# Kernel tuning notes

Measured on AMD Instinct MI355X. Metric: run time of the kernel, lower is better.

## Reference

```python
import jax, jax.numpy as jnp
import numpy as np

N = 20000      # nodes
E = 320000     # edges (avg degree 16)
DIN = 512
DOUT = 512


def setup_inputs() -> dict:
    key = jax.random.key(0)
    ks = jax.random.split(key, 20)
    inp = {}
    inp["X"] = jax.random.normal(ks[0], (N, DIN), jnp.float32)
    inp["edge_index"] = jax.random.randint(ks[1], (2, E), 0, N)
    inp["edge_weight"] = jax.random.uniform(ks[2], (E,), jnp.float32, minval=0.1, maxval=1.0)
    inp["H"] = jax.random.normal(ks[3], (N, DOUT), jnp.float32)
    # six GCNConv layers: x-convs [DIN,DOUT], h-convs [DOUT,DOUT], each with bias [DOUT]
    specs = [("xz", DIN), ("hz", DOUT), ("xr", DIN), ("hr", DOUT), ("xh", DIN), ("hh", DOUT)]
    for i, (tag, din) in enumerate(specs):
        inp[f"W_{tag}"] = jax.random.normal(ks[4 + 2 * i], (din, DOUT), jnp.float32) * 0.05
        inp[f"b_{tag}"] = jax.random.normal(ks[5 + 2 * i], (DOUT,), jnp.float32) * 0.01
    return inp


def _gcn_norm(edge_index, edge_weight, n):
    # PyG gcn_norm: add self-loops (weight 1), symmetric D^-1/2 A D^-1/2
    row, col = edge_index[0], edge_index[1]
    loop = jnp.arange(n, dtype=row.dtype)
    row = jnp.concatenate([row, loop])
    col = jnp.concatenate([col, loop])
    w = jnp.concatenate([edge_weight, jnp.ones((n,), edge_weight.dtype)])
    deg = jax.ops.segment_sum(w, col, num_segments=n)
    dinv = jnp.where(deg > 0, jax.lax.rsqrt(jnp.where(deg > 0, deg, 1.0)), 0.0)
    norm = dinv[row] * w * dinv[col]
    return row, col, norm


def _gcn_conv(x, W, b, row, col, norm, n):
    # out[i] = sum_{j->i} norm_e * (x W)[j] + b
    xw = x @ W                               # [N, DOUT] dense GEMM
    msg = norm[:, None] * xw[row]            # [E+N, DOUT] gather
    return jax.ops.segment_sum(msg, col, num_segments=n) + b


def reference(X, edge_index, edge_weight, H,
              W_xz, b_xz, W_hz, b_hz,
              W_xr, b_xr, W_hr, b_hr,
              W_xh, b_xh, W_hh, b_hh):
    n = X.shape[0]
    row, col, norm = _gcn_norm(edge_index, edge_weight, n)
    conv = lambda x, W, b: _gcn_conv(x, W, b, row, col, norm, n)
    Z = jax.nn.sigmoid(conv(X, W_xz, b_xz) + conv(H, W_hz, b_hz))
    R = jax.nn.sigmoid(conv(X, W_xr, b_xr) + conv(H, W_hr, b_hr))
    H_tilde = jnp.tanh(conv(X, W_xh, b_xh) + conv(H * R, W_hh, b_hh))
    return Z * H + (1.0 - Z) * H_tilde
```

## Files before the change

### kernel.cpp

```cpp
#include <hip/hip_runtime.h>

#define NN 20000
#define NP 20096
#define NE 320000
#define DD 512

typedef __bf16 bf16x8 __attribute__((ext_vector_type(8)));
typedef float f32x4 __attribute__((ext_vector_type(4)));
typedef float f32x2 __attribute__((ext_vector_type(2)));
typedef unsigned short u16;

__device__ __forceinline__ float sigmoidf_(float x) {
  return __builtin_amdgcn_rcpf(1.f + __expf(-x));
}
__device__ __forceinline__ float tanhf_(float x) {
  float xc = fminf(fmaxf(x, -15.f), 15.f);
  float u = __expf(2.f * xc);
  return (u - 1.f) * __builtin_amdgcn_rcpf(u + 1.f);
}

__device__ __forceinline__ unsigned bf16pair(float a, float b) {
  unsigned ua = __builtin_bit_cast(unsigned, a);
  unsigned ub = __builtin_bit_cast(unsigned, b);
  ua = (ua + 0x7FFFu + ((ua >> 16) & 1u)) >> 16;
  ub = (ub + 0x7FFFu + ((ub >> 16) & 1u)) >> 16;
  return ua | (ub << 16);
}
__device__ __forceinline__ u16 bf16one(float a) {
  unsigned ua = __builtin_bit_cast(unsigned, a);
  return (u16)((ua + 0x7FFFu + ((ua >> 16) & 1u)) >> 16);
}
__device__ __forceinline__ float bflo(unsigned w) { return __builtin_bit_cast(float, w << 16); }
__device__ __forceinline__ float bfhi(unsigned w) { return __builtin_bit_cast(float, w & 0xFFFF0000u); }
__device__ __forceinline__ float bf2f(u16 v) { return __builtin_bit_cast(float, (unsigned)v << 16); }

__device__ __forceinline__ void gload16(const void* g, void* l) {
  __builtin_amdgcn_global_load_lds(
      (const __attribute__((address_space(1))) unsigned int*)g,
      (__attribute__((address_space(3))) unsigned int*)l, 16, 0, 0);
}

#define CVT_B 10000
#define INIT_B 79
#define WT_B 1536
__global__ __launch_bounds__(256) void k_setup(
    const float* __restrict__ X, const float* __restrict__ H,
    u16* __restrict__ Xb, u16* __restrict__ Hb,
    const float* __restrict__ W0, const float* __restrict__ W1,
    const float* __restrict__ W2, const float* __restrict__ W3,
    const float* __restrict__ W4, const float* __restrict__ W5,
    u16* __restrict__ T, float* __restrict__ deg, int* __restrict__ cnt) {
  __shared__ float t[32][33];
  int b = blockIdx.x;
  if (b < CVT_B) {
    const int n8 = NN * DD / 8;
    int i = b * 256 + threadIdx.x;
    const float* src = (i < n8) ? X : H;
    u16* dst = (i < n8) ? Xb : Hb;
    int k = (i < n8) ? i : i - n8;
    const float4* s = (const float4*)src;
    float4 v0 = s[k * 2], v1 = s[k * 2 + 1];
    uint4 o = {bf16pair(v0.x, v0.y), bf16pair(v0.z, v0.w),
               bf16pair(v1.x, v1.y), bf16pair(v1.z, v1.w)};
    ((uint4*)dst)[k] = o;
  } else if (b < CVT_B + INIT_B) {
    int i = (b - CVT_B) * 256 + threadIdx.x;
    if (i < NN) { deg[i] = 1.0f; cnt[i] = 0; }
  } else {
    int wb = b - CVT_B - INIT_B;
    const float* Wsrc;
    switch (wb >> 8) {
      case 0: Wsrc = W0; break; case 1: Wsrc = W1; break; case 2: Wsrc = W2; break;
      case 3: Wsrc = W3; break; case 4: Wsrc = W4; break; default: Wsrc = W5; break;
    }
    u16* Wt = T + (size_t)(wb >> 8) * 262144;
    int rb = wb & 255;
    int kb = (rb & 15) * 32, nb = (rb >> 4) * 32;
    int tx = threadIdx.x & 31, ty = threadIdx.x >> 5;
#pragma unroll
    for (int i2 = 0; i2 < 4; ++i2)
      t[ty * 4 + i2][tx] = Wsrc[(size_t)(kb + ty * 4 + i2) * 512 + nb + tx];
    __syncthreads();
#pragma unroll
    for (int i2 = 0; i2 < 4; ++i2)
      Wt[(size_t)(nb + ty * 4 + i2) * 512 + kb + tx] = bf16one(t[tx][ty * 4 + i2]);
  }
}

__global__ void k_accum(const int* col, const float* w, float* deg, int* cnt) {
  int e = blockIdx.x * 256 + threadIdx.x;
  if (e < NE) {
    int c = col[e];
    atomicAdd(&deg[c], w[e]);
    atomicAdd(&cnt[c], 1);
  }
}

__global__ void k_scan(const int* cnt, int* ptr, int* pos) {
  __shared__ int sdata[1024];
  const int ITEMS = (NN + 1023) / 1024;
  int tid = threadIdx.x;
  int base = tid * ITEMS;
  int s = 0;
  for (int j = 0; j < ITEMS; ++j) { int i = base + j; if (i < NN) s += cnt[i]; }
  sdata[tid] = s;
  __syncthreads();
  for (int off = 1; off < 1024; off <<= 1) {
    int v = 0;
    if (tid >= off) v = sdata[tid - off];
    __syncthreads();
    sdata[tid] += v;
    __syncthreads();
  }
  int run = (tid == 0) ? 0 : sdata[tid - 1];
  for (int j = 0; j < ITEMS; ++j) {
    int i = base + j;
    if (i < NN) { ptr[i] = run; pos[i] = run; run += cnt[i]; }
  }
  if (tid == 0) ptr[NN] = NE;
}

__global__ void k_scatter(const int* row, const int* col, const float* w, const float* deg,
                          int* pos, int* erow, float* enorm) {
  int e = blockIdx.x * 256 + threadIdx.x;
  if (e < NE) {
    int r = row[e], c = col[e];
    int slot = atomicAdd(&pos[c], 1);
    erow[slot] = r;
    enorm[slot] = rsqrtf(deg[r]) * w[e] * rsqrtf(deg[c]);
  }
}

#define AGG_B 10000
__global__ __launch_bounds__(256) void k_agg_one(const u16* __restrict__ SA,
                                                 const u16* __restrict__ SB,
                                                 u16* __restrict__ DA,
                                                 u16* __restrict__ DB,
                                                 const int* __restrict__ ptr,
                                                 const int* __restrict__ erow,
                                                 const float* __restrict__ enorm,
                                                 const float* __restrict__ deg) {
  int bid = blockIdx.x;
  bool second = bid >= AGG_B;
  const uint4* S4 = (const uint4*)(second ? SB : SA);
  uint4* D4 = (uint4*)(second ? DB : DA);
  int b = second ? bid - AGG_B : bid;
  int slice = b & 7, nb = b >> 3;
  int w = threadIdx.x >> 6, lane = threadIdx.x & 63;
  int node = nb * 16 + w * 4 + (lane >> 4);
  int q = lane & 15;
  int g = q >> 3, cl = q & 7;
  int soff = slice * 8 + cl;

  float s = rsqrtf(deg[node]), s2 = s * s;
  int pe = ptr[node], e1 = ptr[node + 1];

  f32x2 ax[4] = {};
  auto accum = [&](float nm, uint4 xv) {
    unsigned xw[4] = {xv.x, xv.y, xv.z, xv.w};
    f32x2 nm2 = {nm, nm};
#pragma unroll
    for (int j = 0; j < 4; ++j) {
      f32x2 xf = {bflo(xw[j]), bfhi(xw[j])};
      ax[j] += nm2 * xf;
    }
  };

  if (g == 0) accum(s2, S4[(size_t)node * 64 + soff]);
  int e = pe + 1 - g;
  for (; e + 6 < e1; e += 8) {
    int r0 = erow[e];     float n0 = enorm[e];
    int r1 = erow[e + 2]; float n1 = enorm[e + 2];
    int r2 = erow[e + 4]; float n2 = enorm[e + 4];
    int r3 = erow[e + 6]; float n3 = enorm[e + 6];
    uint4 x0 = S4[(size_t)r0 * 64 + soff];
    uint4 x1 = S4[(size_t)r1 * 64 + soff];
    uint4 x2 = S4[(size_t)r2 * 64 + soff];
    uint4 x3 = S4[(size_t)r3 * 64 + soff];
    accum(n0, x0);
    accum(n1, x1);
    accum(n2, x2);
    accum(n3, x3);
  }
  for (; e < e1; e += 2) accum(enorm[e], S4[(size_t)erow[e] * 64 + soff]);

#pragma unroll
  for (int j = 0; j < 4; ++j) {
    ax[j].x += __shfl_xor(ax[j].x, 8, 64);
    ax[j].y += __shfl_xor(ax[j].y, 8, 64);
  }

  if (g == 0) {
    uint4 ox = {bf16pair(ax[0].x, ax[0].y), bf16pair(ax[1].x, ax[1].y),
                bf16pair(ax[2].x, ax[2].y), bf16pair(ax[3].x, ax[3].y)};
    D4[(size_t)node * 64 + soff] = ox;
  }
}

__global__ __launch_bounds__(256) void k_gemm_big(
    const u16* __restrict__ AXb, const u16* __restrict__ AHb,
    const u16* __restrict__ WtAll,
    const float* __restrict__ bxz, const float* __restrict__ bhz,
    const float* __restrict__ bxr, const float* __restrict__ bhr,
    const u16* __restrict__ Hb,
    u16* __restrict__ Zb, u16* __restrict__ HRb) {
  __shared__ unsigned char smem[32768];
  const int tid = threadIdx.x;
  const int lane = tid & 63, w = tid >> 6;
  const int wr = w >> 1, wc = w & 1;

  const int q = 157;
  const int xcd = blockIdx.x & 7, ii = blockIdx.x >> 3;
  const int wk = xcd * q + ii;
  const int rowBase = (wk >> 3) * 128;
  const int c = wk & 7;
  const int seg = c >> 2;
  const int colBase = (c & 3) * 128;

  const u16* W1 = WtAll + (size_t)(seg ? 2 : 0) * 262144;
  const u16* W2 = WtAll + (size_t)(seg ? 3 : 1) * 262144;

  f32x4 acc[4][4] = {};

  const int lrow = lane & 15;
  const int lkb = (lane >> 4) << 4;
  const int swz = (lane & 7) << 4;
  const int srow = w * 32 + (lane >> 3);
  const int scol = (((lane & 7) ^ (lane >> 3)) << 4);

  for (int pass = 0; pass < 2; ++pass) {
    const u16* A = pass ? AHb : AXb;
    const u16* Wt = pass ? W2 : W1;
    const char* Abase = (const char*)A + (size_t)(rowBase + srow) * 1024 + scol;
    const char* Bbase = (const char*)Wt + (size_t)(colBase + srow) * 1024 + scol;
    for (int k0 = 0; k0 < 512; k0 += 64) {
      __syncthreads();
#pragma unroll
      for (int t = 0; t < 4; ++t) {
        gload16(Abase + (size_t)t * 8192 + k0 * 2, &smem[w * 4096 + t * 1024]);
        gload16(Bbase + (size_t)t * 8192 + k0 * 2, &smem[16384 + w * 4096 + t * 1024]);
      }
      __syncthreads();
#pragma unroll
      for (int ks = 0; ks < 2; ++ks) {
        bf16x8 af[4], bfr[4];
#pragma unroll
        for (int fm = 0; fm < 4; ++fm) {
          int row = wr * 64 + fm * 16 + lrow;
          af[fm] = *(const bf16x8*)&smem[row * 128 + (((ks << 6) + lkb) ^ swz)];
        }
#pragma unroll
        for (int fn = 0; fn < 4; ++fn) {
          int row = wc * 64 + fn * 16 + lrow;
          bfr[fn] = *(const bf16x8*)&smem[16384 + row * 128 + (((ks << 6) + lkb) ^ swz)];
        }
#pragma unroll
        for (int fm = 0; fm < 4; ++fm)
#pragma unroll
          for (int fn = 0; fn < 4; ++fn)
            acc[fm][fn] = __builtin_amdgcn_mfma_f32_16x16x32_bf16(af[fm], bfr[fn], acc[fm][fn], 0, 0, 0);
      }
    }
  }
#pragma unroll
  for (int fm = 0; fm < 4; ++fm) {
    int rbase = rowBase + wr * 64 + fm * 16 + ((lane >> 4) << 2);
#pragma unroll
    for (int fn = 0; fn < 4; ++fn) {
      int col = colBase + wc * 64 + fn * 16 + lrow;
      float bb = seg ? (bxr[col] + bhr[col]) : (bxz[col] + bhz[col]);
#pragma unroll
      for (int r = 0; r < 4; ++r) {
        int row = rbase + r;
        if (row >= NN) continue;
        size_t idx = (size_t)row * 512 + col;
        float a = acc[fm][fn][r] + bb;
        if (seg == 0) {
          Zb[idx] = bf16one(sigmoidf_(a));
        } else {
          HRb[idx] = bf16one(bf2f(Hb[idx]) * sigmoidf_(a));
        }
      }
    }
  }
}

__global__ __launch_bounds__(256) void k_gemm_fin(
    const u16* __restrict__ AHRb, const u16* __restrict__ AXb,
    const u16* __restrict__ WtAll,
    const float* __restrict__ bxh, const float* __restrict__ bhh,
    const u16* __restrict__ Hb, const u16* __restrict__ Zb,
    float* __restrict__ out) {
  __shared__ unsigned char smem[32768];
  const int tid = threadIdx.x;
  const int lane = tid & 63, w = tid >> 6;
  const int wr = w >> 1, wc = w & 1;

  const int q = 78, r8 = 4;
  const int xcd = blockIdx.x & 7, ii = blockIdx.x >> 3;
  const int start = (xcd < r8) ? xcd * (q + 1) : r8 * (q + 1) + (xcd - r8) * q;
  const int wk = start + ii;
  const int rowBase = (wk >> 2) * 128;
  const int colBase = (wk & 3) * 128;

  f32x4 acc[4][4] = {};

  const int lrow = lane & 15;
  const int lkb = (lane >> 4) << 4;
  const int swz = (lane & 7) << 4;
  const int srow = w * 32 + (lane >> 3);
  const int scol = (((lane & 7) ^ (lane >> 3)) << 4);

  for (int pass = 0; pass < 2; ++pass) {
    const u16* A  = pass ? AXb : AHRb;
    const u16* Wt = WtAll + (size_t)(pass ? 4 : 5) * 262144;
    const char* Abase = (const char*)A + (size_t)(rowBase + srow) * 1024 + scol;
    const char* Bbase = (const char*)Wt + (size_t)(colBase + srow) * 1024 + scol;
    for (int k0 = 0; k0 < 512; k0 += 64) {
      __syncthreads();
#pragma unroll
      for (int t = 0; t < 4; ++t) {
        gload16(Abase + (size_t)t * 8192 + k0 * 2, &smem[w * 4096 + t * 1024]);
        gload16(Bbase + (size_t)t * 8192 + k0 * 2, &smem[16384 + w * 4096 + t * 1024]);
      }
      __syncthreads();
#pragma unroll
      for (int ks = 0; ks < 2; ++ks) {
        bf16x8 af[4], bfr[4];
#pragma unroll
        for (int fm = 0; fm < 4; ++fm) {
          int row = wr * 64 + fm * 16 + lrow;
          af[fm] = *(const bf16x8*)&smem[row * 128 + (((ks << 6) + lkb) ^ swz)];
        }
#pragma unroll
        for (int fn = 0; fn < 4; ++fn) {
          int row = wc * 64 + fn * 16 + lrow;
          bfr[fn] = *(const bf16x8*)&smem[16384 + row * 128 + (((ks << 6) + lkb) ^ swz)];
        }
#pragma unroll
        for (int fm = 0; fm < 4; ++fm)
#pragma unroll
          for (int fn = 0; fn < 4; ++fn)
            acc[fm][fn] = __builtin_amdgcn_mfma_f32_16x16x32_bf16(af[fm], bfr[fn], acc[fm][fn], 0, 0, 0);
      }
    }
  }
#pragma unroll
  for (int fm = 0; fm < 4; ++fm) {
    int rbase = rowBase + wr * 64 + fm * 16 + ((lane >> 4) << 2);
#pragma unroll
    for (int fn = 0; fn < 4; ++fn) {
      int col = colBase + wc * 64 + fn * 16 + lrow;
      float bb = bxh[col] + bhh[col];
#pragma unroll
      for (int r = 0; r < 4; ++r) {
        int row = rbase + r;
        if (row >= NN) continue;
        size_t idx = (size_t)row * 512 + col;
        float t = tanhf_(acc[fm][fn][r] + bb);
        float z = bf2f(Zb[idx]);
        float h = bf2f(Hb[idx]);
        out[idx] = z * h + (1.f - z) * t;
      }
    }
  }
}

extern "C" void kernel_launch(void* const* d_in, const int* in_sizes, int n_in,
                              void* d_out, int out_size, void* d_ws, size_t ws_size,
                              hipStream_t stream) {
  const float* X   = (const float*)d_in[0];
  const int*   ei  = (const int*)d_in[1];
  const float* ew  = (const float*)d_in[2];
  const float* H   = (const float*)d_in[3];
  const float* Wxz = (const float*)d_in[4];  const float* bxz = (const float*)d_in[5];
  const float* Whz = (const float*)d_in[6];  const float* bhz = (const float*)d_in[7];
  const float* Wxr = (const float*)d_in[8];  const float* bxr = (const float*)d_in[9];
  const float* Whr = (const float*)d_in[10]; const float* bhr = (const float*)d_in[11];
  const float* Wxh = (const float*)d_in[12]; const float* bxh = (const float*)d_in[13];
  const float* Whh = (const float*)d_in[14]; const float* bhh = (const float*)d_in[15];
  const int* row = ei;
  const int* col = ei + NE;
  float* out = (float*)d_out;

  char* base = (char*)d_ws;
  size_t o = 0;
  auto alloc = [&](size_t b) { char* p = base + o; o += (b + 255) & ~(size_t)255; return p; };
  u16* Xb   = (u16*)alloc((size_t)NP * DD * 2);
  u16* Hb   = (u16*)alloc((size_t)NP * DD * 2);
  u16* AXb  = (u16*)alloc((size_t)NP * DD * 2);
  u16* AHb  = (u16*)alloc((size_t)NP * DD * 2);
  u16* HRb  = (u16*)alloc((size_t)NP * DD * 2);
  u16* Zb   = (u16*)alloc((size_t)NP * DD * 2);
  u16* WtAll= (u16*)alloc((size_t)6 * 512 * 512 * 2);
  float* deg  = (float*)alloc(NN * 4);
  int*   cnt  = (int*)alloc(NN * 4);
  int*   ptr  = (int*)alloc((NN + 1) * 4);
  int*   pos  = (int*)alloc(NN * 4);
  int*   erow = (int*)alloc(NE * 4);
  float* enorm= (float*)alloc(NE * 4);
  u16* AHRb = Xb;

  dim3 b256(256);
  int gE = (NE + 255) / 256;

  k_setup<<<CVT_B + INIT_B + WT_B, b256, 0, stream>>>(
      X, H, Xb, Hb, Wxz, Whz, Wxr, Whr, Wxh, Whh, WtAll, deg, cnt);

  k_accum<<<gE, b256, 0, stream>>>(col, ew, deg, cnt);
  k_scan<<<1, 1024, 0, stream>>>(cnt, ptr, pos);
  k_scatter<<<gE, b256, 0, stream>>>(row, col, ew, deg, pos, erow, enorm);

  k_agg_one<<<2 * AGG_B, b256, 0, stream>>>(Xb, Hb, AXb, AHb, ptr, erow, enorm, deg);

  k_gemm_big<<<1256, b256, 0, stream>>>(AXb, AHb, WtAll, bxz, bhz, bxr, bhr,
                                        Hb, Zb, HRb);

  k_agg_one<<<AGG_B, b256, 0, stream>>>(HRb, HRb, AHRb, AHRb, ptr, erow, enorm, deg);

  k_gemm_fin<<<628, b256, 0, stream>>>(AHRb, AXb, WtAll, bxh, bhh,
                                       Hb, Zb, out);
}
```

Baseline: 320.1 us.

## Interleave aggregated X and H into one K=1024 operand for the fused gate GEMM

The aggregated X and H features now live side by side in one [N,1024] bf16 buffer, and the z/r weights are packed into matching [512,1024] transposed blocks. The gate GEMM then runs a single K=1024 loop instead of two K=512 passes over separate buffers. The final GEMM reads its X half from the interleaved buffer with a 2048-byte row stride. This mainly simplifies the loop structure and removes the pass switch; the total bytes moved stay about the same, and rows of the A and B operands are now spread across a wider stride.

New measurement: 323.1 us. No clear change (+1.0%).

```diff
diff --git a/kernel.cpp b/kernel.cpp
--- a/kernel.cpp
+++ b/kernel.cpp
@@ -39,6 +39,11 @@
       (const __attribute__((address_space(1))) unsigned int*)g,
       (__attribute__((address_space(3))) unsigned int*)l, 16, 0, 0);
 }
+
+#define OFF_WZ 0
+#define OFF_WR 524288
+#define OFF_WXH 1048576
+#define OFF_WHH 1310720
 
 #define CVT_B 10000
 #define INIT_B 79
@@ -68,12 +73,22 @@
     if (i < NN) { deg[i] = 1.0f; cnt[i] = 0; }
   } else {
     int wb = b - CVT_B - INIT_B;
+    int mat = wb >> 8;
     const float* Wsrc;
-    switch (wb >> 8) {
+    switch (mat) {
       case 0: Wsrc = W0; break; case 1: Wsrc = W1; break; case 2: Wsrc = W2; break;
       case 3: Wsrc = W3; break; case 4: Wsrc = W4; break; default: Wsrc = W5; break;
     }
-    u16* Wt = T + (size_t)(wb >> 8) * 262144;
+    u16* dst;
+    int stride, colOff;
+    switch (mat) {
+      case 0: dst = T + OFF_WZ;  stride = 1024; colOff = 0;   break;
+      case 1: dst = T + OFF_WZ;  stride = 1024; colOff = 512; break;
+      case 2: dst = T + OFF_WR;  stride = 1024; colOff = 0;   break;
+      case 3: dst = T + OFF_WR;  stride = 1024; colOff = 512; break;
+      case 4: dst = T + OFF_WXH; stride = 512;  colOff = 0;   break;
+      default: dst = T + OFF_WHH; stride = 512; colOff = 0;   break;
+    }
     int rb = wb & 255;
     int kb = (rb & 15) * 32, nb = (rb >> 4) * 32;
     int tx = threadIdx.x & 31, ty = threadIdx.x >> 5;
@@ -83,7 +98,7 @@
     __syncthreads();
 #pragma unroll
     for (int i2 = 0; i2 < 4; ++i2)
-      Wt[(size_t)(nb + ty * 4 + i2) * 512 + kb + tx] = bf16one(t[tx][ty * 4 + i2]);
+      dst[(size_t)(nb + ty * 4 + i2) * stride + colOff + kb + tx] = bf16one(t[tx][ty * 4 + i2]);
   }
 }
 
@@ -139,7 +154,8 @@
                                                  const int* __restrict__ ptr,
                                                  const int* __restrict__ erow,
                                                  const float* __restrict__ enorm,
-                                                 const float* __restrict__ deg) {
+                                                 const float* __restrict__ deg,
+                                                 int dstride4) {
   int bid = blockIdx.x;
   bool second = bid >= AGG_B;
   const uint4* S4 = (const uint4*)(second ? SB : SA);
@@ -193,13 +209,12 @@
   if (g == 0) {
     uint4 ox = {bf16pair(ax[0].x, ax[0].y), bf16pair(ax[1].x, ax[1].y),
                 bf16pair(ax[2].x, ax[2].y), bf16pair(ax[3].x, ax[3].y)};
-    D4[(size_t)node * 64 + soff] = ox;
+    D4[(size_t)node * dstride4 + soff] = ox;
   }
 }
 
 __global__ __launch_bounds__(256) void k_gemm_big(
-    const u16* __restrict__ AXb, const u16* __restrict__ AHb,
-    const u16* __restrict__ WtAll,
+    const u16* __restrict__ AXH, const u16* __restrict__ WtAll,
     const float* __restrict__ bxz, const float* __restrict__ bhz,
     const float* __restrict__ bxr, const float* __restrict__ bhr,
     const u16* __restrict__ Hb,
@@ -217,8 +232,7 @@
   const int seg = c >> 2;
   const int colBase = (c & 3) * 128;
 
-  const u16* W1 = WtAll + (size_t)(seg ? 2 : 0) * 262144;
-  const u16* W2 = WtAll + (size_t)(seg ? 3 : 1) * 262144;
+  const u16* Wt = WtAll + (seg ? OFF_WR : OFF_WZ);
 
   f32x4 acc[4][4] = {};
 
@@ -228,38 +242,36 @@
   const int srow = w * 32 + (lane >> 3);
   const int scol = (((lane & 7) ^ (lane >> 3)) << 4);
 
-  for (int pass = 0; pass < 2; ++pass) {
-    const u16* A = pass ? AHb : AXb;
-    const u16* Wt = pass ? W2 : W1;
-    const char* Abase = (const char*)A + (size_t)(rowBase + srow) * 1024 + scol;
-    const char* Bbase = (const char*)Wt + (size_t)(colBase + srow) * 1024 + scol;
-    for (int k0 = 0; k0 < 512; k0 += 64) {
-      __syncthreads();
-#pragma unroll
-      for (int t = 0; t < 4; ++t) {
-        gload16(Abase + (size_t)t * 8192 + k0 * 2, &smem[w * 4096 + t * 1024]);
-        gload16(Bbase + (size_t)t * 8192 + k0 * 2, &smem[16384 + w * 4096 + t * 1024]);
-      }
-      __syncthreads();
-#pragma unroll
-      for (int ks = 0; ks < 2; ++ks) {
-        bf16x8 af[4], bfr[4];
-#pragma unroll
-        for (int fm = 0; fm < 4; ++fm) {
-          int row = wr * 64 + fm * 16 + lrow;
-          af[fm] = *(const bf16x8*)&smem[row * 128 + (((ks << 6) + lkb) ^ swz)];
-        }
-#pragma unroll
-        for (int fn = 0; fn < 4; ++fn) {
-          int row = wc * 64 + fn * 16 + lrow;
-          bfr[fn] = *(const bf16x8*)&smem[16384 + row * 128 + (((ks << 6) + lkb) ^ swz)];
-        }
-#pragma unroll
-        for (int fm = 0; fm < 4; ++fm)
-#pragma unroll
-          for (int fn = 0; fn < 4; ++fn)
-            acc[fm][fn] = __builtin_amdgcn_mfma_f32_16x16x32_bf16(af[fm], bfr[fn], acc[fm][fn], 0, 0, 0);
-      }
+  const char* Abase = (const char*)AXH + (size_t)(rowBase + srow) * 2048 + scol;
+  const char* Bbase = (const char*)Wt + (size_t)(colBase + srow) * 2048 + scol;
+
+  for (int kt = 0; kt < 16; ++kt) {
+    size_t ko = (size_t)kt << 7;
+    __syncthreads();
+#pragma unroll
+    for (int t = 0; t < 4; ++t) {
+      gload16(Abase + (size_t)t * 8 * 2048 + ko, &smem[w * 4096 + t * 1024]);
+      gload16(Bbase + (size_t)t * 8 * 2048 + ko, &smem[16384 + w * 4096 + t * 1024]);
+    }
+    __syncthreads();
+#pragma unroll
+    for (int ks = 0; ks < 2; ++ks) {
+      bf16x8 af[4], bfr[4];
+#pragma unroll
+      for (int fm = 0; fm < 4; ++fm) {
+        int row = wr * 64 + fm * 16 + lrow;
+        af[fm] = *(const bf16x8*)&smem[row * 128 + (((ks << 6) + lkb) ^ swz)];
+      }
+#pragma unroll
+      for (int fn = 0; fn < 4; ++fn) {
+        int row = wc * 64 + fn * 16 + lrow;
+        bfr[fn] = *(const bf16x8*)&smem[16384 + row * 128 + (((ks << 6) + lkb) ^ swz)];
+      }
+#pragma unroll
+      for (int fm = 0; fm < 4; ++fm)
+#pragma unroll
+        for (int fn = 0; fn < 4; ++fn)
+          acc[fm][fn] = __builtin_amdgcn_mfma_f32_16x16x32_bf16(af[fm], bfr[fn], acc[fm][fn], 0, 0, 0);
     }
   }
 #pragma unroll
@@ -286,7 +298,7 @@
 }
 
 __global__ __launch_bounds__(256) void k_gemm_fin(
-    const u16* __restrict__ AHRb, const u16* __restrict__ AXb,
+    const u16* __restrict__ AHRb, const u16* __restrict__ AXH,
     const u16* __restrict__ WtAll,
     const float* __restrict__ bxh, const float* __restrict__ bhh,
     const u16* __restrict__ Hb, const u16* __restrict__ Zb,
@@ -312,16 +324,24 @@
   const int scol = (((lane & 7) ^ (lane >> 3)) << 4);
 
   for (int pass = 0; pass < 2; ++pass) {
-    const u16* A  = pass ? AXb : AHRb;
-    const u16* Wt = WtAll + (size_t)(pass ? 4 : 5) * 262144;
-    const char* Abase = (const char*)A + (size_t)(rowBase + srow) * 1024 + scol;
+    const char* Abase;
+    size_t strideA;
+    if (pass == 0) {
+      Abase = (const char*)AHRb + (size_t)(rowBase + srow) * 1024 + scol;
+      strideA = 1024;
+    } else {
+      Abase = (const char*)AXH + (size_t)(rowBase + srow) * 2048 + scol;
+      strideA = 2048;
+    }
+    const u16* Wt = WtAll + (pass ? OFF_WXH : OFF_WHH);
     const char* Bbase = (const char*)Wt + (size_t)(colBase + srow) * 1024 + scol;
-    for (int k0 = 0; k0 < 512; k0 += 64) {
+    for (int kt = 0; kt < 8; ++kt) {
+      size_t ko = (size_t)kt << 7;
       __syncthreads();
 #pragma unroll
       for (int t = 0; t < 4; ++t) {
-        gload16(Abase + (size_t)t * 8192 + k0 * 2, &smem[w * 4096 + t * 1024]);
-        gload16(Bbase + (size_t)t * 8192 + k0 * 2, &smem[16384 + w * 4096 + t * 1024]);
+        gload16(Abase + (size_t)t * 8 * strideA + ko, &smem[w * 4096 + t * 1024]);
+        gload16(Bbase + (size_t)t * 8 * 1024 + ko, &smem[16384 + w * 4096 + t * 1024]);
       }
       __syncthreads();
 #pragma unroll
@@ -388,8 +408,7 @@
   auto alloc = [&](size_t b) { char* p = base + o; o += (b + 255) & ~(size_t)255; return p; };
   u16* Xb   = (u16*)alloc((size_t)NP * DD * 2);
   u16* Hb   = (u16*)alloc((size_t)NP * DD * 2);
-  u16* AXb  = (u16*)alloc((size_t)NP * DD * 2);
-  u16* AHb  = (u16*)alloc((size_t)NP * DD * 2);
+  u16* AXH  = (u16*)alloc((size_t)NP * 1024 * 2);
   u16* HRb  = (u16*)alloc((size_t)NP * DD * 2);
   u16* Zb   = (u16*)alloc((size_t)NP * DD * 2);
   u16* WtAll= (u16*)alloc((size_t)6 * 512 * 512 * 2);
@@ -411,13 +430,15 @@
   k_scan<<<1, 1024, 0, stream>>>(cnt, ptr, pos);
   k_scatter<<<gE, b256, 0, stream>>>(row, col, ew, deg, pos, erow, enorm);
 
-  k_agg_one<<<2 * AGG_B, b256, 0, stream>>>(Xb, Hb, AXb, AHb, ptr, erow, enorm, deg);
-
-  k_gemm_big<<<1256, b256, 0, stream>>>(AXb, AHb, WtAll, bxz, bhz, bxr, bhr,
+  k_agg_one<<<2 * AGG_B, b256, 0, stream>>>(Xb, Hb, AXH, AXH + 512,
+                                            ptr, erow, enorm, deg, 128);
+
+  k_gemm_big<<<1256, b256, 0, stream>>>(AXH, WtAll, bxz, bhz, bxr, bhr,
                                         Hb, Zb, HRb);
 
-  k_agg_one<<<AGG_B, b256, 0, stream>>>(HRb, HRb, AHRb, AHRb, ptr, erow, enorm, deg);
-
-  k_gemm_fin<<<628, b256, 0, stream>>>(AHRb, AXb, WtAll, bxh, bhh,
+  k_agg_one<<<AGG_B, b256, 0, stream>>>(HRb, HRb, AHRb, AHRb,
+                                        ptr, erow, enorm, deg, 64);
+
+  k_gemm_fin<<<628, b256, 0, stream>>>(AHRb, AXH, WtAll, bxh, bhh,
                                        Hb, Zb, out);
 }
```
